# Performance work log

Hardware: AMD Instinct MI355X
Metric: run time of the kernel (lower is better)

Reference implementation:

```python
import jax, jax.numpy as jnp
import numpy as np
from jax import lax

DIM = 192
HEADS = 4
HIDDEN = int(DIM * 2.66)  # 510
B, H, W = 2, 64, 64
EPS_LN = 1e-6
EPS_NORM = 1e-12


def conv1x1(x, w, b):
    # x: (b,c,h,w), w: (o,c), b: (o,)
    return jnp.einsum('bchw,oc->bohw', x, w) + b[None, :, None, None]


def dwconv3x3(x, w, b):
    # depthwise 3x3, SAME padding; w: (C,1,3,3)
    c = x.shape[1]
    y = lax.conv_general_dilated(x, w, window_strides=(1, 1), padding='SAME',
                                 feature_group_count=c,
                                 dimension_numbers=('NCHW', 'OIHW', 'NCHW'))
    return y + b[None, :, None, None]


def layernorm2d(x, w, b):
    mean = jnp.mean(x, axis=(2, 3), keepdims=True)
    var = jnp.mean((x - mean) ** 2, axis=(2, 3), keepdims=True)
    return (x - mean) / jnp.sqrt(var + EPS_LN) * w[None, :, None, None] + b[None, :, None, None]


def mdta(x, qkv_w, qkv_b, qkv_dw_w, qkv_dw_b, temperature, proj_w, proj_b):
    b, c, h, w = x.shape
    qkv = dwconv3x3(conv1x1(x, qkv_w, qkv_b), qkv_dw_w, qkv_dw_b)
    q, k, v = jnp.split(qkv, 3, axis=1)
    dh = c // HEADS
    q = q.reshape(b, HEADS, dh, h * w)
    k = k.reshape(b, HEADS, dh, h * w)
    v = v.reshape(b, HEADS, dh, h * w)
    # L2-normalize over per-head channel dim (axis=2), like F.normalize(dim=2)
    q = q / jnp.maximum(jnp.linalg.norm(q, axis=2, keepdims=True), EPS_NORM)
    k = k / jnp.maximum(jnp.linalg.norm(k, axis=2, keepdims=True), EPS_NORM)
    # spatial attention map: (b, heads, HW, HW)
    attn = jnp.einsum('bhcn,bhcm->bhnm', q, k) * temperature[None]  # temp (heads,1,1)
    attn = jax.nn.softmax(attn, axis=-1)
    out = jnp.einsum('bhnm,bhcm->bhcn', attn, v)  # (b,heads,dh,HW)
    out = out.reshape(b, c, h, w)
    return conv1x1(out, proj_w, proj_b)


def gdfn(x, pin_w, pin_b, dw_w, dw_b, pout_w, pout_b):
    y = dwconv3x3(conv1x1(x, pin_w, pin_b), dw_w, dw_b)
    y1, y2 = jnp.split(y, 2, axis=1)
    y = jax.nn.gelu(y1, approximate=False) * y2
    return conv1x1(y, pout_w, pout_b)


def setup_inputs() -> dict:
    key = jax.random.key(0)
    ks = jax.random.split(key, 8)
    s = 0.02
    return {
        'x': jax.random.normal(ks[0], (B, DIM, H, W), jnp.float32),
        'ln1_w': jnp.ones((DIM,), jnp.float32),
        'ln1_b': jnp.zeros((DIM,), jnp.float32),
        'qkv_w': jax.random.normal(ks[1], (DIM * 3, DIM), jnp.float32) * s,
        'qkv_b': jnp.zeros((DIM * 3,), jnp.float32),
        'qkv_dw_w': jax.random.normal(ks[2], (DIM * 3, 1, 3, 3), jnp.float32) * s,
        'qkv_dw_b': jnp.zeros((DIM * 3,), jnp.float32),
        'temperature': jnp.ones((HEADS, 1, 1), jnp.float32),
        'proj_w': jax.random.normal(ks[3], (DIM, DIM), jnp.float32) * s,
        'proj_b': jnp.zeros((DIM,), jnp.float32),
        'ln2_w': jnp.ones((DIM,), jnp.float32),
        'ln2_b': jnp.zeros((DIM,), jnp.float32),
        'pin_w': jax.random.normal(ks[4], (HIDDEN * 2, DIM), jnp.float32) * s,
        'pin_b': jnp.zeros((HIDDEN * 2,), jnp.float32),
        'gdfn_dw_w': jax.random.normal(ks[5], (HIDDEN * 2, 1, 3, 3), jnp.float32) * s,
        'gdfn_dw_b': jnp.zeros((HIDDEN * 2,), jnp.float32),
        'pout_w': jax.random.normal(ks[6], (DIM, HIDDEN), jnp.float32) * s,
        'pout_b': jnp.zeros((DIM,), jnp.float32),
    }


def reference(x, ln1_w, ln1_b, qkv_w, qkv_b, qkv_dw_w, qkv_dw_b, temperature,
              proj_w, proj_b, ln2_w, ln2_b, pin_w, pin_b, gdfn_dw_w, gdfn_dw_b,
              pout_w, pout_b):
    x = x + mdta(layernorm2d(x, ln1_w, ln1_b), qkv_w, qkv_b, qkv_dw_w, qkv_dw_b,
                 temperature, proj_w, proj_b)
    x = x + gdfn(layernorm2d(x, ln2_w, ln2_b), pin_w, pin_b, gdfn_dw_w, gdfn_dw_b,
                 pout_w, pout_b)
    return x
```

## Files before the change

kernel.cpp:

```cpp
#include <hip/hip_runtime.h>
#include <hip/hip_bf16.h>

typedef __bf16 bf16x8 __attribute__((ext_vector_type(8)));
typedef __bf16 bf16x4 __attribute__((ext_vector_type(4)));
typedef __bf16 bf16x2 __attribute__((ext_vector_type(2)));
typedef float f32x4 __attribute__((ext_vector_type(4)));

#define HW 4096
#define DIMC 192
#define DH 48
#define HIDC 510
#define LOG2E 1.44269504088896f

__device__ __forceinline__ float exp2_fast(float x) {
#if __has_builtin(__builtin_amdgcn_exp2f)
  return __builtin_amdgcn_exp2f(x);
#else
  float r;
  asm("v_exp_f32 %0, %1\n\ts_nop 1" : "=v"(r) : "v"(x));
  return r;
#endif
}

__device__ __forceinline__ float rcp_fast(float x) {
#if __has_builtin(__builtin_amdgcn_rcpf)
  return __builtin_amdgcn_rcpf(x);
#else
  float r;
  asm("v_rcp_f32 %0, %1\n\ts_nop 1" : "=v"(r) : "v"(x));
  return r;
#endif
}

__device__ __forceinline__ float gelu_fast(float x) {
  float z = fabsf(x) * 0.70710678118654752f;
  float t = rcp_fast(fmaf(0.3275911f, z, 1.f));
  float p = t * fmaf(t, fmaf(t, fmaf(t, fmaf(t, 1.061405429f, -1.453152027f), 1.421413741f), -0.284496736f), 0.254829592f);
  float e = exp2_fast(-z * z * 1.4426950408889634f);
  float erfa = 1.f - p * e;
  float erfx = copysignf(erfa, x);
  return 0.5f * x * (1.f + erfx);
}

__global__ void wcvt4_kernel(const float* __restrict__ qkv_w, const float* __restrict__ proj_w,
                             const float* __restrict__ pin_w, const float* __restrict__ pout_w,
                             __bf16* __restrict__ wb_qkv, __bf16* __restrict__ wb_proj,
                             __bf16* __restrict__ wb_pin, __bf16* __restrict__ wb_pout) {
  int idx = blockIdx.x * 256 + threadIdx.x;
  if (idx < 110592) {
    wb_qkv[idx] = (__bf16)qkv_w[idx];
  } else if (idx < 147456) {
    int i = idx - 110592;
    wb_proj[i] = (__bf16)proj_w[i];
  } else if (idx < 343296) {
    int i = idx - 147456;
    wb_pin[i] = (__bf16)pin_w[i];
  } else if (idx < 441600) {
    int i = idx - 343296;
    int o = i >> 9, c = i & 511;
    wb_pout[i] = (c < HIDC) ? (__bf16)pout_w[o * HIDC + c] : (__bf16)0.f;
  }
}

__global__ __launch_bounds__(256) void ln_stats_kernel(const float* __restrict__ x, const float* __restrict__ w,
                                                       const float* __restrict__ b, float* __restrict__ sc,
                                                       float* __restrict__ sh) {
  int bc = blockIdx.x;
  int c = bc % DIMC;
  const float* row = x + (size_t)bc * HW;
  float s = 0.f, s2 = 0.f;
  for (int i = threadIdx.x * 4; i < HW; i += 1024) {
    f32x4 v = *(const f32x4*)&row[i];
    s += (v.x + v.y) + (v.z + v.w);
    s2 = fmaf(v.x, v.x, s2); s2 = fmaf(v.y, v.y, s2);
    s2 = fmaf(v.z, v.z, s2); s2 = fmaf(v.w, v.w, s2);
  }
  __shared__ float red[8];
  for (int off = 32; off; off >>= 1) { s += __shfl_down(s, off, 64); s2 += __shfl_down(s2, off, 64); }
  int wid = threadIdx.x >> 6;
  if ((threadIdx.x & 63) == 0) { red[wid] = s; red[4 + wid] = s2; }
  __syncthreads();
  if (threadIdx.x == 0) {
    s = red[0] + red[1] + red[2] + red[3];
    s2 = red[4] + red[5] + red[6] + red[7];
    float mean = s * (1.f / HW);
    float var = s2 * (1.f / HW) - mean * mean;
    float rstd = rsqrtf(var + 1e-6f);
    float scv = rstd * w[c];
    sc[bc] = scv;
    sh[bc] = b[c] - mean * scv;
  }
}

__global__ __launch_bounds__(256) void ln_apply_t_kernel(const float* __restrict__ x, const float* __restrict__ sc,
                                                         const float* __restrict__ sh, __bf16* __restrict__ Xt) {
  int n0 = blockIdx.x * 64, c0 = blockIdx.y * 32, b = blockIdx.z;
  int t = threadIdx.x;
  int n = t & 63, cs = c0 + (t >> 6) * 8;
  __bf16 ob[8];
#pragma unroll
  for (int cc = 0; cc < 8; ++cc) {
    int c = cs + cc;
    float v = fmaf(x[((size_t)(b * DIMC + c)) * HW + n0 + n], sc[b * DIMC + c], sh[b * DIMC + c]);
    ob[cc] = (__bf16)v;
  }
  *(bf16x8*)&Xt[((size_t)((b << 12) + n0 + n)) * DIMC + cs] = *(bf16x8*)ob;
}

__global__ __launch_bounds__(256) void gemm_kernel(const __bf16* __restrict__ A, const __bf16* __restrict__ Bt,
                                                   const float* __restrict__ bias, const float* __restrict__ res,
                                                   float* __restrict__ outf, __bf16* __restrict__ outb,
                                                   int O, int Cs, int mode) {
  __shared__ __align__(16) __bf16 Asub[64 * 72];
  __shared__ __align__(16) __bf16 Bsub[128 * 72];
  const int t = threadIdx.x;
  const int lane = t & 63, wv = t >> 6;
  const int q4 = lane >> 4, l16 = lane & 15;
  int o0 = blockIdx.y * 64;
  if (o0 + 64 > O) o0 = O - 64;
  const int ntot0 = blockIdx.x * 128;
  const int b = ntot0 >> 12;
  const int n_in_b0 = ntot0 & 4095;

  f32x4 acc[8];
#pragma unroll
  for (int nt = 0; nt < 8; ++nt) acc[nt] = (f32x4){0.f, 0.f, 0.f, 0.f};

  for (int c0 = 0; c0 < Cs; c0 += 64) {
    __syncthreads();
#pragma unroll
    for (int j = 0; j < 2; ++j) {
      int id = t + 256 * j;
      *(bf16x8*)&Asub[(id >> 3) * 72 + (id & 7) * 8] =
          *(const bf16x8*)&A[((size_t)(o0 + (id >> 3))) * Cs + c0 + (id & 7) * 8];
    }
    if (mode != 3) {
#pragma unroll
      for (int j = 0; j < 4; ++j) {
        int id = t + 256 * j;
        *(bf16x8*)&Bsub[(id >> 3) * 72 + (id & 7) * 8] =
            *(const bf16x8*)&Bt[((size_t)(ntot0 + (id >> 3))) * Cs + c0 + (id & 7) * 8];
      }
    } else {
      int cr = t & 63, seg = t >> 6;
      int cg = c0 + cr;
      __bf16 tmp[32];
      if (cg < HIDC) {
        const __bf16* gp = Bt + ((size_t)(b * HIDC + cg)) * HW + n_in_b0 + seg * 32;
#pragma unroll
        for (int j = 0; j < 4; ++j) *(bf16x8*)&tmp[8 * j] = *(const bf16x8*)&gp[8 * j];
      } else {
#pragma unroll
        for (int k = 0; k < 32; ++k) tmp[k] = (__bf16)0.f;
      }
#pragma unroll
      for (int k = 0; k < 32; ++k) Bsub[(seg * 32 + k) * 72 + cr] = tmp[k];
    }
    __syncthreads();
#pragma unroll
    for (int ks = 0; ks < 2; ++ks) {
      bf16x8 af = *(const bf16x8*)&Asub[(16 * wv + l16) * 72 + 32 * ks + 8 * q4];
#pragma unroll
      for (int nt = 0; nt < 8; ++nt) {
        bf16x8 bfr = *(const bf16x8*)&Bsub[(16 * nt + l16) * 72 + 32 * ks + 8 * q4];
        acc[nt] = __builtin_amdgcn_mfma_f32_16x16x32_bf16(af, bfr, acc[nt], 0, 0, 0);
      }
    }
  }

  float bvals[4];
#pragma unroll
  for (int r = 0; r < 4; ++r) bvals[r] = bias[o0 + 16 * wv + 4 * q4 + r];
#pragma unroll
  for (int nt = 0; nt < 8; ++nt) {
    int n_in_b = n_in_b0 + 16 * nt + l16;
#pragma unroll
    for (int r = 0; r < 4; ++r) {
      int o = o0 + 16 * wv + 4 * q4 + r;
      size_t addr = ((size_t)(b * O + o)) * HW + n_in_b;
      float v = acc[nt][r] + bvals[r];
      if (mode >= 2) { outf[addr] = v + res[addr]; }
      else if (mode == 0) { outf[addr] = v; }
      else { outb[addr] = (__bf16)v; }
    }
  }
}

__global__ __launch_bounds__(256) void dwconv_split_kernel(const __bf16* __restrict__ in, const float* __restrict__ w,
                                                           const float* __restrict__ bias,
                                                           __bf16* __restrict__ qdwb, __bf16* __restrict__ Vbf) {
  int bc = blockIdx.x;
  int b = bc / 576, ch = bc - b * 576;
  __shared__ float tile[66 * 68];
  for (int i = threadIdx.x; i < 66 * 68; i += 256) tile[i] = 0.f;
  __syncthreads();
  const __bf16* p = in + (size_t)bc * HW;
  for (int j = 0; j < 8; ++j) {
    int i = 2 * threadIdx.x + 512 * j;
    bf16x2 v = *(const bf16x2*)&p[i];
    int y = i >> 6, xx = i & 63;
    tile[(y + 1) * 68 + xx + 1] = (float)v.x;
    tile[(y + 1) * 68 + xx + 2] = (float)v.y;
  }
  __syncthreads();
  float w0 = w[ch * 9 + 0], w1 = w[ch * 9 + 1], w2 = w[ch * 9 + 2];
  float w3 = w[ch * 9 + 3], w4 = w[ch * 9 + 4], w5 = w[ch * 9 + 5];
  float w6 = w[ch * 9 + 6], w7 = w[ch * 9 + 7], w8 = w[ch * 9 + 8];
  float bb = bias[ch];
  __bf16* dst;
  if (ch < 384) dst = qdwb + ((size_t)(b * 384 + ch)) * HW;
  else {
    int c = ch - 384, h = c / DH, cc = c - h * DH;
    dst = Vbf + ((size_t)((b * 4 + h) * DH + cc)) * HW;
  }
  for (int j = 0; j < 8; ++j) {
    int i = 2 * threadIdx.x + 512 * j;
    int y = i >> 6, xx = i & 63;
    const float* tt = &tile[y * 68 + xx];
    float a = bb;
    a = fmaf(w0, tt[0], a);   a = fmaf(w1, tt[1], a);   a = fmaf(w2, tt[2], a);
    a = fmaf(w3, tt[68], a);  a = fmaf(w4, tt[69], a);  a = fmaf(w5, tt[70], a);
    a = fmaf(w6, tt[136], a); a = fmaf(w7, tt[137], a); a = fmaf(w8, tt[138], a);
    float a2 = bb;
    a2 = fmaf(w0, tt[1], a2);   a2 = fmaf(w1, tt[2], a2);   a2 = fmaf(w2, tt[3], a2);
    a2 = fmaf(w3, tt[69], a2);  a2 = fmaf(w4, tt[70], a2);  a2 = fmaf(w5, tt[71], a2);
    a2 = fmaf(w6, tt[137], a2); a2 = fmaf(w7, tt[138], a2); a2 = fmaf(w8, tt[139], a2);
    bf16x2 o = { (__bf16)a, (__bf16)a2 };
    *(bf16x2*)&dst[i] = o;
  }
}

__global__ __launch_bounds__(256) void gdfn_dw_gate_kernel(const __bf16* __restrict__ hid, const float* __restrict__ w,
                                                           const float* __restrict__ bias, __bf16* __restrict__ gate) {
  int blk = blockIdx.x;
  int b = blk / HIDC, j = blk - b * HIDC;
  __shared__ __align__(16) float t1[66 * 68];
  __shared__ __align__(16) float t2[66 * 68];
  const int tid = threadIdx.x;
  if (tid < 136) {
    int r = (tid >= 68) ? 65 : 0;
    int c = (tid >= 68) ? tid - 68 : tid;
    t1[r * 68 + c] = 0.f;
    t2[r * 68 + c] = 0.f;
  }
  {
    int r = (tid >> 2) + 1;
    int c4 = tid & 3;
    int c = (c4 == 0) ? 0 : 64 + c4;
    t1[r * 68 + c] = 0.f;
    t2[r * 68 + c] = 0.f;
  }
  const __bf16* p1 = hid + ((size_t)b * (2 * HIDC) + j) * HW;
  const __bf16* p2 = p1 + (size_t)HIDC * HW;
  for (int jj = 0; jj < 8; ++jj) {
    int i = 2 * tid + 512 * jj;
    bf16x2 v1 = *(const bf16x2*)&p1[i];
    bf16x2 v2 = *(const bf16x2*)&p2[i];
    int y = i >> 6, xx = i & 63;
    t1[(y + 1) * 68 + xx + 1] = (float)v1.x;
    t1[(y + 1) * 68 + xx + 2] = (float)v1.y;
    t2[(y + 1) * 68 + xx + 1] = (float)v2.x;
    t2[(y + 1) * 68 + xx + 2] = (float)v2.y;
  }
  __syncthreads();
  int c1 = j, c2 = j + HIDC;
  float wa[9], wb[9];
#pragma unroll
  for (int k = 0; k < 9; ++k) { wa[k] = w[c1 * 9 + k]; wb[k] = w[c2 * 9 + k]; }
  float bi1 = bias[c1], bi2 = bias[c2];

  const int y = tid >> 2, x0 = 16 * (tid & 3);
  float x1v[16], x2v[16];
#pragma unroll
  for (int p = 0; p < 16; ++p) { x1v[p] = bi1; x2v[p] = bi2; }
#pragma unroll
  for (int r = 0; r < 3; ++r) {
    const float* rp1 = &t1[(y + r) * 68 + x0];
    float rr[20];
#pragma unroll
    for (int q = 0; q < 5; ++q) *(f32x4*)&rr[4 * q] = *(const f32x4*)&rp1[4 * q];
    float w0 = wa[3 * r], w1 = wa[3 * r + 1], w2 = wa[3 * r + 2];
#pragma unroll
    for (int p = 0; p < 16; ++p)
      x1v[p] = fmaf(w0, rr[p], fmaf(w1, rr[p + 1], fmaf(w2, rr[p + 2], x1v[p])));
  }
#pragma unroll
  for (int r = 0; r < 3; ++r) {
    const float* rp2 = &t2[(y + r) * 68 + x0];
    float rr[20];
#pragma unroll
    for (int q = 0; q < 5; ++q) *(f32x4*)&rr[4 * q] = *(const f32x4*)&rp2[4 * q];
    float w0 = wb[3 * r], w1 = wb[3 * r + 1], w2 = wb[3 * r + 2];
#pragma unroll
    for (int p = 0; p < 16; ++p)
      x2v[p] = fmaf(w0, rr[p], fmaf(w1, rr[p + 1], fmaf(w2, rr[p + 2], x2v[p])));
  }
  __bf16 ob[16];
#pragma unroll
  for (int p = 0; p < 16; ++p) ob[p] = (__bf16)(gelu_fast(x1v[p]) * x2v[p]);
  __bf16* op = gate + ((size_t)b * HIDC + j) * HW + y * 64 + x0;
  *(bf16x8*)&op[0] = *(bf16x8*)&ob[0];
  *(bf16x8*)&op[8] = *(bf16x8*)&ob[8];
}

__global__ __launch_bounds__(256) void prep_qk_kernel(const __bf16* __restrict__ qdwb, const float* __restrict__ temp,
                                                      __bf16* __restrict__ Qbf, __bf16* __restrict__ Kbf) {
  int t2 = blockIdx.x * 256 + threadIdx.x;
  int bh = t2 >> 11;
  int np = (t2 & 2047) * 2;
  int b = bh >> 2, h = bh & 3;
  const int isK = blockIdx.y;
  const __bf16* sp = qdwb + ((size_t)(b * 384 + isK * 192 + h * DH)) * HW + np;
  float tq = isK ? 1.f : temp[h] * LOG2E;

  bf16x2 raw[DH];
  float ss0 = 0.f, ss1 = 0.f;
#pragma unroll
  for (int c = 0; c < DH; ++c) {
    bf16x2 v = *(const bf16x2*)&sp[(size_t)c * HW];
    raw[c] = v;
    float f0 = (float)v.x, f1 = (float)v.y;
    ss0 = fmaf(f0, f0, ss0);
    ss1 = fmaf(f1, f1, ss1);
  }
  float sc0 = tq / fmaxf(sqrtf(ss0), 1e-12f);
  float sc1 = tq / fmaxf(sqrtf(ss1), 1e-12f);
  __bf16 ob0[64], ob1[64];
#pragma unroll
  for (int c = 0; c < DH; ++c) {
    ob0[c] = (__bf16)((float)raw[c].x * sc0);
    ob1[c] = (__bf16)((float)raw[c].y * sc1);
  }
#pragma unroll
  for (int c = DH; c < 64; ++c) { ob0[c] = (__bf16)0.f; ob1[c] = (__bf16)0.f; }
  __bf16* dd = (isK ? Kbf : Qbf) + ((size_t)(bh << 12) + np) * 64;
#pragma unroll
  for (int ch = 0; ch < 8; ++ch) {
    *(bf16x8*)&dd[ch * 8] = *(bf16x8*)&ob0[ch * 8];
    *(bf16x8*)&dd[64 + ch * 8] = *(bf16x8*)&ob1[ch * 8];
  }
}

__global__ __launch_bounds__(256) void attn_split_kernel(const __bf16* __restrict__ Qbf, const __bf16* __restrict__ Kbf,
                                                         const __bf16* __restrict__ Vbf, float* __restrict__ part) {
  __shared__ __align__(16) __bf16 Vc[2][48 * 72];
  __shared__ __align__(16) __bf16 Pl[2][64 * 72];
  const int tid = threadIdx.x;
  const int lane = tid & 63;
  const int wv = tid >> 6;
  const int q4 = lane >> 4, l16 = lane & 15;
  const int bid = blockIdx.x;
  const int chunk = bid >> 9, rest = bid & 511;
  const int bh = rest >> 6, nt = rest & 63;
  const int n0 = nt * 64;
  const __bf16* Qg = Qbf + (size_t)bh * HW * 64;
  const __bf16* Kg = Kbf + (size_t)bh * HW * 64;
  const __bf16* Vg = Vbf + (size_t)bh * DH * HW;

  bf16x8 qf[4][2];
#pragma unroll
  for (int s = 0; s < 4; ++s)
#pragma unroll
    for (int ks = 0; ks < 2; ++ks)
      qf[s][ks] = *(const bf16x8*)&Qg[((size_t)(n0 + 16 * s + l16)) * 64 + 32 * ks + 8 * q4];

  const int m0 = chunk * 2048;
  bf16x8 kf0 = *(const bf16x8*)&Kg[((size_t)(m0 + 16 * wv + l16)) * 64 + 8 * q4];
  bf16x8 kf1 = *(const bf16x8*)&Kg[((size_t)(m0 + 16 * wv + l16)) * 64 + 32 + 8 * q4];
  bf16x8 vreg[2];
  vreg[0] = *(const bf16x8*)&Vg[((size_t)(tid >> 3)) * HW + m0 + (tid & 7) * 8];
  if (tid < 128) {
    int i = tid + 256;
    vreg[1] = *(const bf16x8*)&Vg[((size_t)(i >> 3)) * HW + m0 + (i & 7) * 8];
  }

  float lsub[4] = {0.f, 0.f, 0.f, 0.f};
  f32x4 oacc[3];
#pragma unroll
  for (int ct = 0; ct < 3; ++ct) oacc[ct] = (f32x4){0.f, 0.f, 0.f, 0.f};

  const int mt_end = chunk * 32 + 32;
  for (int mt = chunk * 32; mt < mt_end; ++mt) {
    const int cur = mt & 1;
    *(bf16x8*)&Vc[cur][(tid >> 3) * 72 + (tid & 7) * 8] = vreg[0];
    if (tid < 128) {
      int i = tid + 256;
      *(bf16x8*)&Vc[cur][(i >> 3) * 72 + (i & 7) * 8] = vreg[1];
    }
    const int m1 = (mt + 1 < mt_end) ? (mt + 1) * 64 : mt * 64;
    bf16x8 kn0 = *(const bf16x8*)&Kg[((size_t)(m1 + 16 * wv + l16)) * 64 + 8 * q4];
    bf16x8 kn1 = *(const bf16x8*)&Kg[((size_t)(m1 + 16 * wv + l16)) * 64 + 32 + 8 * q4];
    vreg[0] = *(const bf16x8*)&Vg[((size_t)(tid >> 3)) * HW + m1 + (tid & 7) * 8];
    if (tid < 128) {
      int i = tid + 256;
      vreg[1] = *(const bf16x8*)&Vg[((size_t)(i >> 3)) * HW + m1 + (i & 7) * 8];
    }

    f32x4 sacc[4];
#pragma unroll
    for (int s = 0; s < 4; ++s) sacc[s] = (f32x4){0.f, 0.f, 0.f, 0.f};
    __builtin_amdgcn_s_setprio(1);
#pragma unroll
    for (int s = 0; s < 4; ++s)
      sacc[s] = __builtin_amdgcn_mfma_f32_16x16x32_bf16(kf0, qf[s][0], sacc[s], 0, 0, 0);
#pragma unroll
    for (int s = 0; s < 4; ++s)
      sacc[s] = __builtin_amdgcn_mfma_f32_16x16x32_bf16(kf1, qf[s][1], sacc[s], 0, 0, 0);
    __builtin_amdgcn_s_setprio(0);

#pragma unroll
    for (int s = 0; s < 4; ++s) {
      float p0 = exp2_fast(sacc[s][0]);
      float p1 = exp2_fast(sacc[s][1]);
      float p2 = exp2_fast(sacc[s][2]);
      float p3 = exp2_fast(sacc[s][3]);
      lsub[s] += (p0 + p1) + (p2 + p3);
      bf16x4 pk = { (__bf16)p0, (__bf16)p1, (__bf16)p2, (__bf16)p3 };
      *(bf16x4*)&Pl[cur][(16 * s + l16) * 72 + 16 * wv + 4 * q4] = pk;
    }
    __syncthreads();

    __builtin_amdgcn_s_setprio(1);
#pragma unroll
    for (int ks = 0; ks < 2; ++ks) {
      bf16x8 pf = *(const bf16x8*)&Pl[cur][(16 * wv + l16) * 72 + 32 * ks + 8 * q4];
#pragma unroll
      for (int ct = 0; ct < 3; ++ct) {
        bf16x8 vf = *(const bf16x8*)&Vc[cur][(16 * ct + l16) * 72 + 32 * ks + 8 * q4];
        oacc[ct] = __builtin_amdgcn_mfma_f32_16x16x32_bf16(pf, vf, oacc[ct], 0, 0, 0);
      }
    }
    __builtin_amdgcn_s_setprio(0);
    kf0 = kn0; kf1 = kn1;
  }

  __syncthreads();
  float* Lred = (float*)&Pl[0][0];
#pragma unroll
  for (int s = 0; s < 4; ++s) {
    float v = lsub[s];
    v += __shfl_xor(v, 16, 64);
    v += __shfl_xor(v, 32, 64);
    if (q4 == 0) Lred[wv * 64 + 16 * s + l16] = v;
  }
  __syncthreads();
  size_t pbase = (size_t)bid * 3136;
  if (tid < 64)
    part[pbase + 3072 + tid] = Lred[tid] + Lred[64 + tid] + Lred[128 + tid] + Lred[192 + tid];
#pragma unroll
  for (int ct = 0; ct < 3; ++ct)
#pragma unroll
    for (int r = 0; r < 4; ++r) {
      int n = 16 * wv + 4 * q4 + r;
      part[pbase + (size_t)n * 48 + 16 * ct + l16] = oacc[ct][r];
    }
}

__global__ __launch_bounds__(256) void attn_merge_kernel(const float* __restrict__ part, __bf16* __restrict__ Xt) {
  const int bid = blockIdx.x;
  const int bh = bid >> 6, nt = bid & 63;
  const int b = bh >> 2, h = bh & 3;
  const int n0 = nt * 64;
  const int t = threadIdx.x;
  __shared__ float linv[64];
  if (t < 64) {
    float s = 0.f;
#pragma unroll
    for (int ch = 0; ch < 2; ++ch) s += part[((size_t)(ch * 512 + bid)) * 3136 + 3072 + t];
    linv[t] = rcp_fast(s);
  }
  __syncthreads();
#pragma unroll
  for (int j = 0; j < 3; ++j) {
    int id = t + 256 * j;
    int n = id / 12, cc = (id - n * 12) * 4;
    f32x4 s = (f32x4){0.f, 0.f, 0.f, 0.f};
#pragma unroll
    for (int ch = 0; ch < 2; ++ch) s += *(const f32x4*)&part[((size_t)(ch * 512 + bid)) * 3136 + (size_t)n * 48 + cc];
    float li = linv[n];
    bf16x4 ov = { (__bf16)(s.x * li), (__bf16)(s.y * li), (__bf16)(s.z * li), (__bf16)(s.w * li) };
    *(bf16x4*)&Xt[((size_t)((b << 12) + n0 + n)) * DIMC + h * DH + cc] = ov;
  }
}

extern "C" void kernel_launch(void* const* d_in, const int* in_sizes, int n_in,
                              void* d_out, int out_size, void* d_ws, size_t ws_size,
                              hipStream_t stream) {
  const float* x        = (const float*)d_in[0];
  const float* ln1_w    = (const float*)d_in[1];
  const float* ln1_b    = (const float*)d_in[2];
  const float* qkv_w    = (const float*)d_in[3];
  const float* qkv_b    = (const float*)d_in[4];
  const float* qkv_dw_w = (const float*)d_in[5];
  const float* qkv_dw_b = (const float*)d_in[6];
  const float* temperature = (const float*)d_in[7];
  const float* proj_w   = (const float*)d_in[8];
  const float* proj_b   = (const float*)d_in[9];
  const float* ln2_w    = (const float*)d_in[10];
  const float* ln2_b    = (const float*)d_in[11];
  const float* pin_w    = (const float*)d_in[12];
  const float* pin_b    = (const float*)d_in[13];
  const float* gdfn_dw_w = (const float*)d_in[14];
  const float* gdfn_dw_b = (const float*)d_in[15];
  const float* pout_w   = (const float*)d_in[16];
  const float* pout_b   = (const float*)d_in[17];
  float* out = (float*)d_out;
  float* ws = (float*)d_ws;

  __bf16* wb_qkv  = (__bf16*)(ws + 0);
  __bf16* wb_proj = (__bf16*)(ws + 55296);
  __bf16* wb_pin  = (__bf16*)(ws + 73728);
  __bf16* wb_pout = (__bf16*)(ws + 171648);
  float* sc1 = ws + 220800;
  float* sh1 = ws + 221184;
  float* sc2 = ws + 221568;
  float* sh2 = ws + 221952;
  __bf16* Xt1 = (__bf16*)(ws + 222336);
  __bf16* Xt2 = (__bf16*)(ws + 222336);
  __bf16* Qbf = (__bf16*)(ws + 222336);
  __bf16* Kbf = (__bf16*)(ws + 1270912);
  __bf16* Vbf = (__bf16*)(ws + 2319488);
  __bf16* qkvb   = (__bf16*)(ws + 3105920);
  __bf16* Xt_att = (__bf16*)(ws + 3105920);
  __bf16* hid    = (__bf16*)(ws + 3105920);
  __bf16* qdwb  = (__bf16*)(ws + 5465216);
  float*  Opart = ws + 5465216;
  __bf16* gate  = (__bf16*)(ws + 7283840);

  wcvt4_kernel<<<1725, 256, 0, stream>>>(qkv_w, proj_w, pin_w, pout_w, wb_qkv, wb_proj, wb_pin, wb_pout);

  ln_stats_kernel<<<2 * DIMC, 256, 0, stream>>>(x, ln1_w, ln1_b, sc1, sh1);
  ln_apply_t_kernel<<<dim3(64, 6, 2), 256, 0, stream>>>(x, sc1, sh1, Xt1);
  gemm_kernel<<<dim3(64, 9), 256, 0, stream>>>(wb_qkv, Xt1, qkv_b, nullptr, nullptr, qkvb, 576, 192, 1);
  dwconv_split_kernel<<<1152, 256, 0, stream>>>(qkvb, qkv_dw_w, qkv_dw_b, qdwb, Vbf);
  prep_qk_kernel<<<dim3(64, 2), 256, 0, stream>>>(qdwb, temperature, Qbf, Kbf);
  attn_split_kernel<<<1024, 256, 0, stream>>>(Qbf, Kbf, Vbf, Opart);
  attn_merge_kernel<<<512, 256, 0, stream>>>(Opart, Xt_att);
  gemm_kernel<<<dim3(64, 3), 256, 0, stream>>>(wb_proj, Xt_att, proj_b, x, out, nullptr, 192, 192, 2);

  ln_stats_kernel<<<2 * DIMC, 256, 0, stream>>>(out, ln2_w, ln2_b, sc2, sh2);
  ln_apply_t_kernel<<<dim3(64, 6, 2), 256, 0, stream>>>(out, sc2, sh2, Xt2);
  gemm_kernel<<<dim3(64, 16), 256, 0, stream>>>(wb_pin, Xt2, pin_b, nullptr, nullptr, hid, 1020, 192, 1);
  gdfn_dw_gate_kernel<<<2 * HIDC, 256, 0, stream>>>(hid, gdfn_dw_w, gdfn_dw_b, gate);
  gemm_kernel<<<dim3(64, 3), 256, 0, stream>>>(wb_pout, (const __bf16*)gate, pout_b, out, out, nullptr, 192, 512, 3);
}
```

Before: 241.3 us.

## Fuse attention merge into proj GEMM and weight-convert with LN1 stats

Removes the attn_merge kernel by adding a GEMM mode that reads the two fp32 attention partials, normalizes them by the summed softmax denominators, and writes bf16 tiles straight into shared memory. This drops a launch and the round trip of the intermediate Xt_att buffer. The weight-conversion and first LayerNorm-stats kernels are merged into one launch with block-index dispatch. The attention loop also switches to incrementing pointers, which drops the clamped last-iteration prefetch and may read one tile past the chunk. In exchange, the three proj GEMM column blocks each re-read and re-reduce the fp32 partials.

Measured after the change: 238.2 us, median of 2. No clear change (-1.3%).

```diff
diff --git a/kernel.cpp b/kernel.cpp
--- a/kernel.cpp
+++ b/kernel.cpp
@@ -42,23 +42,54 @@
   return 0.5f * x * (1.f + erfx);
 }
 
-__global__ void wcvt4_kernel(const float* __restrict__ qkv_w, const float* __restrict__ proj_w,
-                             const float* __restrict__ pin_w, const float* __restrict__ pout_w,
-                             __bf16* __restrict__ wb_qkv, __bf16* __restrict__ wb_proj,
-                             __bf16* __restrict__ wb_pin, __bf16* __restrict__ wb_pout) {
-  int idx = blockIdx.x * 256 + threadIdx.x;
-  if (idx < 110592) {
-    wb_qkv[idx] = (__bf16)qkv_w[idx];
-  } else if (idx < 147456) {
-    int i = idx - 110592;
-    wb_proj[i] = (__bf16)proj_w[i];
-  } else if (idx < 343296) {
-    int i = idx - 147456;
-    wb_pin[i] = (__bf16)pin_w[i];
-  } else if (idx < 441600) {
-    int i = idx - 343296;
-    int o = i >> 9, c = i & 511;
-    wb_pout[i] = (c < HIDC) ? (__bf16)pout_w[o * HIDC + c] : (__bf16)0.f;
+__global__ __launch_bounds__(256) void wcvt_ln_kernel(const float* __restrict__ qkv_w, const float* __restrict__ proj_w,
+                                                      const float* __restrict__ pin_w, const float* __restrict__ pout_w,
+                                                      __bf16* __restrict__ wb_qkv, __bf16* __restrict__ wb_proj,
+                                                      __bf16* __restrict__ wb_pin, __bf16* __restrict__ wb_pout,
+                                                      const float* __restrict__ x, const float* __restrict__ lw,
+                                                      const float* __restrict__ lb, float* __restrict__ sc,
+                                                      float* __restrict__ sh) {
+  __shared__ float red[8];
+  if (blockIdx.x < 1725) {
+    int idx = blockIdx.x * 256 + threadIdx.x;
+    if (idx < 110592) {
+      wb_qkv[idx] = (__bf16)qkv_w[idx];
+    } else if (idx < 147456) {
+      int i = idx - 110592;
+      wb_proj[i] = (__bf16)proj_w[i];
+    } else if (idx < 343296) {
+      int i = idx - 147456;
+      wb_pin[i] = (__bf16)pin_w[i];
+    } else if (idx < 441600) {
+      int i = idx - 343296;
+      int o = i >> 9, c = i & 511;
+      wb_pout[i] = (c < HIDC) ? (__bf16)pout_w[o * HIDC + c] : (__bf16)0.f;
+    }
+    return;
+  }
+  int bc = blockIdx.x - 1725;
+  int c = bc % DIMC;
+  const float* row = x + (size_t)bc * HW;
+  float s = 0.f, s2 = 0.f;
+  for (int i = threadIdx.x * 4; i < HW; i += 1024) {
+    f32x4 v = *(const f32x4*)&row[i];
+    s += (v.x + v.y) + (v.z + v.w);
+    s2 = fmaf(v.x, v.x, s2); s2 = fmaf(v.y, v.y, s2);
+    s2 = fmaf(v.z, v.z, s2); s2 = fmaf(v.w, v.w, s2);
+  }
+  for (int off = 32; off; off >>= 1) { s += __shfl_down(s, off, 64); s2 += __shfl_down(s2, off, 64); }
+  int wid = threadIdx.x >> 6;
+  if ((threadIdx.x & 63) == 0) { red[wid] = s; red[4 + wid] = s2; }
+  __syncthreads();
+  if (threadIdx.x == 0) {
+    s = red[0] + red[1] + red[2] + red[3];
+    s2 = red[4] + red[5] + red[6] + red[7];
+    float mean = s * (1.f / HW);
+    float var = s2 * (1.f / HW) - mean * mean;
+    float rstd = rsqrtf(var + 1e-6f);
+    float scv = rstd * lw[c];
+    sc[bc] = scv;
+    sh[bc] = lb[c] - mean * scv;
   }
 }
 
@@ -110,9 +141,11 @@
 __global__ __launch_bounds__(256) void gemm_kernel(const __bf16* __restrict__ A, const __bf16* __restrict__ Bt,
                                                    const float* __restrict__ bias, const float* __restrict__ res,
                                                    float* __restrict__ outf, __bf16* __restrict__ outb,
+                                                   const float* __restrict__ part,
                                                    int O, int Cs, int mode) {
   __shared__ __align__(16) __bf16 Asub[64 * 72];
   __shared__ __align__(16) __bf16 Bsub[128 * 72];
+  __shared__ float linvS[4][128];
   const int t = threadIdx.x;
   const int lane = t & 63, wv = t >> 6;
   const int q4 = lane >> 4, l16 = lane & 15;
@@ -122,6 +155,19 @@
   const int b = ntot0 >> 12;
   const int n_in_b0 = ntot0 & 4095;
 
+  if (mode == 4) {
+#pragma unroll
+    for (int jj = 0; jj < 2; ++jj) {
+      int id = t + 256 * jj;
+      int h = id >> 7, nl = id & 127;
+      int n_in_b = n_in_b0 + nl;
+      int ntb = n_in_b >> 6, n64 = n_in_b & 63;
+      size_t pb = ((size_t)((b * 4 + h) * 64 + ntb)) * 3136 + 3072 + n64;
+      float s = part[pb] + part[pb + (size_t)512 * 3136];
+      linvS[h][nl] = rcp_fast(s);
+    }
+  }
+
   f32x4 acc[8];
 #pragma unroll
   for (int nt = 0; nt < 8; ++nt) acc[nt] = (f32x4){0.f, 0.f, 0.f, 0.f};
@@ -134,7 +180,29 @@
       *(bf16x8*)&Asub[(id >> 3) * 72 + (id & 7) * 8] =
           *(const bf16x8*)&A[((size_t)(o0 + (id >> 3))) * Cs + c0 + (id & 7) * 8];
     }
-    if (mode != 3) {
+    if (mode == 4) {
+#pragma unroll
+      for (int j = 0; j < 4; ++j) {
+        int id = t + 256 * j;
+        int row = id >> 3, cgrp = id & 7;
+        int cglob = c0 + cgrp * 8;
+        int h = cglob / 48;
+        int cc = cglob - h * 48;
+        int n_in_b = n_in_b0 + row;
+        int ntb = n_in_b >> 6, n64 = n_in_b & 63;
+        size_t pb = ((size_t)((b * 4 + h) * 64 + ntb)) * 3136 + (size_t)n64 * 48 + cc;
+        f32x4 a0 = *(const f32x4*)&part[pb];
+        f32x4 a1 = *(const f32x4*)&part[pb + 4];
+        f32x4 b0 = *(const f32x4*)&part[pb + (size_t)512 * 3136];
+        f32x4 b1 = *(const f32x4*)&part[pb + (size_t)512 * 3136 + 4];
+        float li = linvS[h][row];
+        f32x4 s0 = (a0 + b0) * li;
+        f32x4 s1 = (a1 + b1) * li;
+        bf16x8 ov = { (__bf16)s0.x, (__bf16)s0.y, (__bf16)s0.z, (__bf16)s0.w,
+                      (__bf16)s1.x, (__bf16)s1.y, (__bf16)s1.z, (__bf16)s1.w };
+        *(bf16x8*)&Bsub[row * 72 + cgrp * 8] = ov;
+      }
+    } else if (mode != 3) {
 #pragma unroll
       for (int j = 0; j < 4; ++j) {
         int id = t + 256 * j;
@@ -365,36 +433,33 @@
       qf[s][ks] = *(const bf16x8*)&Qg[((size_t)(n0 + 16 * s + l16)) * 64 + 32 * ks + 8 * q4];
 
   const int m0 = chunk * 2048;
-  bf16x8 kf0 = *(const bf16x8*)&Kg[((size_t)(m0 + 16 * wv + l16)) * 64 + 8 * q4];
-  bf16x8 kf1 = *(const bf16x8*)&Kg[((size_t)(m0 + 16 * wv + l16)) * 64 + 32 + 8 * q4];
+  const __bf16* kp0 = Kg + ((size_t)(m0 + 16 * wv + l16)) * 64 + 8 * q4;
+  const __bf16* kp1 = kp0 + 32;
+  const __bf16* vp0 = Vg + ((size_t)(tid >> 3)) * HW + m0 + (tid & 7) * 8;
+  const __bf16* vp1 = Vg + ((size_t)((tid + 256) >> 3)) * HW + m0 + ((tid + 256) & 7) * 8;
+  bf16x8 kf0 = *(const bf16x8*)kp0;
+  bf16x8 kf1 = *(const bf16x8*)kp1;
   bf16x8 vreg[2];
-  vreg[0] = *(const bf16x8*)&Vg[((size_t)(tid >> 3)) * HW + m0 + (tid & 7) * 8];
-  if (tid < 128) {
-    int i = tid + 256;
-    vreg[1] = *(const bf16x8*)&Vg[((size_t)(i >> 3)) * HW + m0 + (i & 7) * 8];
-  }
+  vreg[0] = *(const bf16x8*)vp0;
+  if (tid < 128) vreg[1] = *(const bf16x8*)vp1;
 
   float lsub[4] = {0.f, 0.f, 0.f, 0.f};
   f32x4 oacc[3];
 #pragma unroll
   for (int ct = 0; ct < 3; ++ct) oacc[ct] = (f32x4){0.f, 0.f, 0.f, 0.f};
 
-  const int mt_end = chunk * 32 + 32;
-  for (int mt = chunk * 32; mt < mt_end; ++mt) {
-    const int cur = mt & 1;
+  for (int it = 0; it < 32; ++it) {
+    const int cur = it & 1;
     *(bf16x8*)&Vc[cur][(tid >> 3) * 72 + (tid & 7) * 8] = vreg[0];
     if (tid < 128) {
       int i = tid + 256;
       *(bf16x8*)&Vc[cur][(i >> 3) * 72 + (i & 7) * 8] = vreg[1];
     }
-    const int m1 = (mt + 1 < mt_end) ? (mt + 1) * 64 : mt * 64;
-    bf16x8 kn0 = *(const bf16x8*)&Kg[((size_t)(m1 + 16 * wv + l16)) * 64 + 8 * q4];
-    bf16x8 kn1 = *(const bf16x8*)&Kg[((size_t)(m1 + 16 * wv + l16)) * 64 + 32 + 8 * q4];
-    vreg[0] = *(const bf16x8*)&Vg[((size_t)(tid >> 3)) * HW + m1 + (tid & 7) * 8];
-    if (tid < 128) {
-      int i = tid + 256;
-      vreg[1] = *(const bf16x8*)&Vg[((size_t)(i >> 3)) * HW + m1 + (i & 7) * 8];
-    }
+    kp0 += 4096; kp1 += 4096; vp0 += 64; vp1 += 64;
+    bf16x8 kn0 = *(const bf16x8*)kp0;
+    bf16x8 kn1 = *(const bf16x8*)kp1;
+    vreg[0] = *(const bf16x8*)vp0;
+    if (tid < 128) vreg[1] = *(const bf16x8*)vp1;
 
     f32x4 sacc[4];
 #pragma unroll
@@ -454,33 +519,6 @@
       int n = 16 * wv + 4 * q4 + r;
       part[pbase + (size_t)n * 48 + 16 * ct + l16] = oacc[ct][r];
     }
-}
-
-__global__ __launch_bounds__(256) void attn_merge_kernel(const float* __restrict__ part, __bf16* __restrict__ Xt) {
-  const int bid = blockIdx.x;
-  const int bh = bid >> 6, nt = bid & 63;
-  const int b = bh >> 2, h = bh & 3;
-  const int n0 = nt * 64;
-  const int t = threadIdx.x;
-  __shared__ float linv[64];
-  if (t < 64) {
-    float s = 0.f;
-#pragma unroll
-    for (int ch = 0; ch < 2; ++ch) s += part[((size_t)(ch * 512 + bid)) * 3136 + 3072 + t];
-    linv[t] = rcp_fast(s);
-  }
-  __syncthreads();
-#pragma unroll
-  for (int j = 0; j < 3; ++j) {
-    int id = t + 256 * j;
-    int n = id / 12, cc = (id - n * 12) * 4;
-    f32x4 s = (f32x4){0.f, 0.f, 0.f, 0.f};
-#pragma unroll
-    for (int ch = 0; ch < 2; ++ch) s += *(const f32x4*)&part[((size_t)(ch * 512 + bid)) * 3136 + (size_t)n * 48 + cc];
-    float li = linv[n];
-    bf16x4 ov = { (__bf16)(s.x * li), (__bf16)(s.y * li), (__bf16)(s.z * li), (__bf16)(s.w * li) };
-    *(bf16x4*)&Xt[((size_t)((b << 12) + n0 + n)) * DIMC + h * DH + cc] = ov;
-  }
 }
 
 extern "C" void kernel_launch(void* const* d_in, const int* in_sizes, int n_in,
@@ -521,26 +559,24 @@
   __bf16* Kbf = (__bf16*)(ws + 1270912);
   __bf16* Vbf = (__bf16*)(ws + 2319488);
   __bf16* qkvb   = (__bf16*)(ws + 3105920);
-  __bf16* Xt_att = (__bf16*)(ws + 3105920);
   __bf16* hid    = (__bf16*)(ws + 3105920);
   __bf16* qdwb  = (__bf16*)(ws + 5465216);
   float*  Opart = ws + 5465216;
   __bf16* gate  = (__bf16*)(ws + 7283840);
 
-  wcvt4_kernel<<<1725, 256, 0, stream>>>(qkv_w, proj_w, pin_w, pout_w, wb_qkv, wb_proj, wb_pin, wb_pout);
-
-  ln_stats_kernel<<<2 * DIMC, 256, 0, stream>>>(x, ln1_w, ln1_b, sc1, sh1);
+  wcvt_ln_kernel<<<1725 + 2 * DIMC, 256, 0, stream>>>(qkv_w, proj_w, pin_w, pout_w,
+                                                      wb_qkv, wb_proj, wb_pin, wb_pout,
+                                                      x, ln1_w, ln1_b, sc1, sh1);
   ln_apply_t_kernel<<<dim3(64, 6, 2), 256, 0, stream>>>(x, sc1, sh1, Xt1);
-  gemm_kernel<<<dim3(64, 9), 256, 0, stream>>>(wb_qkv, Xt1, qkv_b, nullptr, nullptr, qkvb, 576, 192, 1);
+  gemm_kernel<<<dim3(64, 9), 256, 0, stream>>>(wb_qkv, Xt1, qkv_b, nullptr, nullptr, qkvb, nullptr, 576, 192, 1);
   dwconv_split_kernel<<<1152, 256, 0, stream>>>(qkvb, qkv_dw_w, qkv_dw_b, qdwb, Vbf);
   prep_qk_kernel<<<dim3(64, 2), 256, 0, stream>>>(qdwb, temperature, Qbf, Kbf);
   attn_split_kernel<<<1024, 256, 0, stream>>>(Qbf, Kbf, Vbf, Opart);
-  attn_merge_kernel<<<512, 256, 0, stream>>>(Opart, Xt_att);
-  gemm_kernel<<<dim3(64, 3), 256, 0, stream>>>(wb_proj, Xt_att, proj_b, x, out, nullptr, 192, 192, 2);
+  gemm_kernel<<<dim3(64, 3), 256, 0, stream>>>(wb_proj, nullptr, proj_b, x, out, nullptr, Opart, 192, 192, 4);
 
   ln_stats_kernel<<<2 * DIMC, 256, 0, stream>>>(out, ln2_w, ln2_b, sc2, sh2);
   ln_apply_t_kernel<<<dim3(64, 6, 2), 256, 0, stream>>>(out, sc2, sh2, Xt2);
-  gemm_kernel<<<dim3(64, 16), 256, 0, stream>>>(wb_pin, Xt2, pin_b, nullptr, nullptr, hid, 1020, 192, 1);
+  gemm_kernel<<<dim3(64, 16), 256, 0, stream>>>(wb_pin, Xt2, pin_b, nullptr, nullptr, hid, nullptr, 1020, 192, 1);
   gdfn_dw_gate_kernel<<<2 * HIDC, 256, 0, stream>>>(hid, gdfn_dw_w, gdfn_dw_b, gate);
-  gemm_kernel<<<dim3(64, 3), 256, 0, stream>>>(wb_pout, (const __bf16*)gate, pout_b, out, out, nullptr, 192, 512, 3);
-}
+  gemm_kernel<<<dim3(64, 3), 256, 0, stream>>>(wb_pout, (const __bf16*)gate, pout_b, out, out, nullptr, nullptr, 192, 512, 3);
+}
```
